# Kernel optimization log

Measured on AMD Instinct MI355X. Metric: run time of the kernel, lower is better.

The kernel has to match this reference:

```python
import jax, jax.numpy as jnp
import numpy as np

GROUP_SIZE = 128

def dequantize(imatrix, scales, zeros, group_size, out_dtype):
    # repeat group-wise scales/zeros along axis 0 to full weight shape
    rs = jnp.repeat(scales, group_size, axis=0)
    rz = jnp.repeat(zeros, group_size, axis=0)
    return ((imatrix.astype(rs.dtype) - rz.astype(rs.dtype)) * rs).astype(out_dtype)

def setup_inputs() -> dict:
    key = jax.random.key(0)
    ks = jax.random.split(key, 10)
    H, I, G = 4096, 14336, GROUP_SIZE
    B, S = 4, 2048
    x = jax.random.normal(ks[0], (B, S, H), dtype=jnp.float32)
    gate_w = jax.random.randint(ks[1], (H, I), 0, 16, dtype=jnp.int32)
    gate_z = jax.random.randint(ks[2], (H // G, I), 0, 16, dtype=jnp.int32)
    gate_s = jax.random.uniform(ks[3], (H // G, I), dtype=jnp.float32) * 0.01
    up_w = jax.random.randint(ks[4], (H, I), 0, 16, dtype=jnp.int32)
    up_z = jax.random.randint(ks[5], (H // G, I), 0, 16, dtype=jnp.int32)
    up_s = jax.random.uniform(ks[6], (H // G, I), dtype=jnp.float32) * 0.01
    down_w = jax.random.randint(ks[7], (I, H), 0, 16, dtype=jnp.int32)
    down_z = jax.random.randint(ks[8], (I // G, H), 0, 16, dtype=jnp.int32)
    down_s = jax.random.uniform(ks[9], (I // G, H), dtype=jnp.float32) * 0.01
    return {"x": x, "gate_w": gate_w, "gate_z": gate_z, "gate_s": gate_s,
            "up_w": up_w, "up_z": up_z, "up_s": up_s,
            "down_w": down_w, "down_z": down_z, "down_s": down_s}

def reference(x, gate_w, gate_z, gate_s, up_w, up_z, up_s, down_w, down_z, down_s):
    dt = x.dtype
    gate_proj = dequantize(gate_w, gate_s, gate_z, GROUP_SIZE, dt)  # [H, I]
    up_proj = dequantize(up_w, up_s, up_z, GROUP_SIZE, dt)          # [H, I]
    down_proj = dequantize(down_w, down_s, down_z, GROUP_SIZE, dt)  # [I, H]
    gate = jax.nn.silu(jnp.dot(x, gate_proj))  # [B, S, I]
    up = jnp.dot(x, up_proj)                   # [B, S, I]
    return jnp.dot(gate * up, down_proj)       # [B, S, H]
```

## Files before the change

### kernel.cpp

```cpp
#include <hip/hip_runtime.h>
#include <cstdint>
#include <cstddef>

typedef unsigned short u16;
typedef unsigned int u32;
typedef float f32x4 __attribute__((ext_vector_type(4)));
typedef __bf16 bf16x8 __attribute__((ext_vector_type(8)));

__device__ inline u16 f32_to_bf16(float f) {
  u32 u = __float_as_uint(f);
  u = (u + 0x7FFFu + ((u >> 16) & 1u)) >> 16;
  return (u16)u;
}

#define GLD16(src, dst)                                                        \
  __builtin_amdgcn_global_load_lds(                                            \
      (const __attribute__((address_space(1))) u32*)(src),                     \
      (__attribute__((address_space(3))) u32*)(dst), 16, 0, 0)

#define SBAR() __builtin_amdgcn_s_barrier()
#define SETPRIO(x) __builtin_amdgcn_s_setprio(x)
#define WAIT_LGKM0()                                                           \
  do {                                                                         \
    asm volatile("s_waitcnt lgkmcnt(0)" ::: "memory");                         \
    __builtin_amdgcn_sched_barrier(0);                                         \
  } while (0)
#define WAITV(N) asm volatile("s_waitcnt vmcnt(" #N ")" ::: "memory")
#define MFMA16(a, b, c) __builtin_amdgcn_mfma_f32_16x16x32_bf16(a, b, c, 0, 0, 0)

__device__ inline void stage_op(const char* src, void* ldsBase, int rowBase,
                                int wave) {
  GLD16(src, (char*)ldsBase + rowBase * 128 + wave * 1024);
}

__device__ inline bf16x8 fragK(const u16* tile, int row, int ks, int p) {
  const int byte = row * 128 + (((ks << 6) + (p << 4)) ^ ((row & 7) << 4));
  return *(const bf16x8*)((const char*)tile + byte);
}

__global__ void k_convert_x(const float* __restrict__ x, u16* __restrict__ o) {
  const long i = (long)blockIdx.x * 256 + threadIdx.x;
  const float4 a = ((const float4*)x)[i * 2];
  const float4 b = ((const float4*)x)[i * 2 + 1];
  uint4 r;
  r.x = (u32)f32_to_bf16(a.x) | ((u32)f32_to_bf16(a.y) << 16);
  r.y = (u32)f32_to_bf16(a.z) | ((u32)f32_to_bf16(a.w) << 16);
  r.z = (u32)f32_to_bf16(b.x) | ((u32)f32_to_bf16(b.y) << 16);
  r.w = (u32)f32_to_bf16(b.z) | ((u32)f32_to_bf16(b.w) << 16);
  ((uint4*)o)[i] = r;
}

__global__ __launch_bounds__(256) void k_dequant(const int* __restrict__ W,
                                                 const int* __restrict__ Z,
                                                 const float* __restrict__ S,
                                                 u16* __restrict__ out, int K,
                                                 int N) {
  __shared__ u16 ldsT[256 * 66];
  const int k0 = blockIdx.x * 64, n0 = blockIdx.y * 256;
  const int t = threadIdx.x;
  const int n4 = t & 63;
  const int kr = t >> 6;
  const int g = k0 >> 7;
  const int nb = n0 + n4 * 4;
  const int4 z4 = *(const int4*)(Z + (size_t)g * N + nb);
  const float4 s4 = *(const float4*)(S + (size_t)g * N + nb);
#pragma unroll
  for (int pass = 0; pass < 16; ++pass) {
    const int kl = kr + pass * 4;
    const int4 w4 = *(const int4*)(W + (size_t)(k0 + kl) * N + nb);
    ldsT[(n4 * 4 + 0) * 66 + kl] = f32_to_bf16((float)(w4.x - z4.x) * s4.x);
    ldsT[(n4 * 4 + 1) * 66 + kl] = f32_to_bf16((float)(w4.y - z4.y) * s4.y);
    ldsT[(n4 * 4 + 2) * 66 + kl] = f32_to_bf16((float)(w4.z - z4.z) * s4.z);
    ldsT[(n4 * 4 + 3) * 66 + kl] = f32_to_bf16((float)(w4.w - z4.w) * s4.w);
  }
  __syncthreads();
#pragma unroll
  for (int pass = 0; pass < 8; ++pass) {
    const int nl = pass * 32 + (t >> 3);
    const int kc = (t & 7) * 8;
    const u16* p = &ldsT[nl * 66 + kc];
    const u32 w0 = *(const u32*)(p + 0);
    const u32 w1 = *(const u32*)(p + 2);
    const u32 w2 = *(const u32*)(p + 4);
    const u32 w3 = *(const u32*)(p + 6);
    *(uint4*)(out + (size_t)(n0 + nl) * K + k0 + kc) =
        make_uint4(w0, w1, w2, w3);
  }
}

__global__ __launch_bounds__(512, 2) void k_gemm_gu(
    const u16* __restrict__ X, const u16* __restrict__ WG,
    const u16* __restrict__ WU, u16* __restrict__ Hout) {
  __shared__ __align__(16) u16 lA[2][16384];
  __shared__ __align__(16) u16 lG[2][8192];
  __shared__ __align__(16) u16 lU[2][8192];
  const int NT = 896;
  const int m0 = blockIdx.x * 256;
  const int ng = blockIdx.y;
  const int tid = threadIdx.x, lane = tid & 63, wave = tid >> 6;
  const int p = lane >> 4, r16 = lane & 15;
  const int wr = wave >> 2, wc = wave & 3;

  const int srow = tid >> 3;
  const int skb = (((tid ^ (tid >> 3)) & 7) << 4);
  const char* baA = (const char*)X + (long)(m0 + srow) * 8192 + skb;
  const char* baG = (const char*)WG + (long)srow * 8192 + skb;
  const char* baU = (const char*)WU + (long)srow * 8192 + skb;

#define NROW(t2) ((long)((ng + 8 * ((t2) >> 6)) << 7))
#define KBYTE(t2) (((t2) & 63) * 128)
#define ISS_A(t2, rb) \
  stage_op(baA + (long)(rb) * 8192 + KBYTE(t2), lA[(t2) & 1], rb, wave)
#define ISS_G(t2, rb) \
  stage_op(baG + (NROW(t2) + (rb)) * 8192 + KBYTE(t2), lG[(t2) & 1], rb, wave)
#define ISS_U(t2, rb) \
  stage_op(baU + (NROW(t2) + (rb)) * 8192 + KBYTE(t2), lU[(t2) & 1], rb, wave)

  f32x4 aG[8][2], aU[8][2];
  const f32x4 zero = {0.f, 0.f, 0.f, 0.f};
#pragma unroll
  for (int i = 0; i < 8; ++i)
#pragma unroll
    for (int j = 0; j < 2; ++j) {
      aG[i][j] = zero;
      aU[i][j] = zero;
    }

  ISS_A(0, 0); ISS_A(0, 128); ISS_G(0, 0); ISS_G(0, 64);
  ISS_U(0, 0); ISS_U(0, 64); ISS_A(0, 64); ISS_A(0, 192);
  ISS_A(1, 0); ISS_A(1, 128);
  WAITV(6);
  SBAR();

  for (int r = 0; r < 14; ++r) {
    for (int kt = 0; kt < 64; ++kt) {
      const int t = r * 64 + kt;
      const int b = kt & 1;
      const u16* hA = lA[b];
      const u16* hG = lG[b];
      const u16* hU = lU[b];
      bf16x8 af[2][4], gf[2][2], uf[2][2];
#pragma unroll
      for (int ks = 0; ks < 2; ++ks) {
#pragma unroll
        for (int ii = 0; ii < 4; ++ii)
          af[ks][ii] = fragK(hA, wr * 128 + ii * 16 + r16, ks, p);
#pragma unroll
        for (int j = 0; j < 2; ++j)
          gf[ks][j] = fragK(hG, wc * 32 + j * 16 + r16, ks, p);
      }
      if (t < NT - 1) { ISS_G(t + 1, 0); ISS_G(t + 1, 64); }
      SBAR();
      WAIT_LGKM0();
      SETPRIO(1);
#pragma unroll
      for (int ks = 0; ks < 2; ++ks)
#pragma unroll
        for (int ii = 0; ii < 4; ++ii)
#pragma unroll
          for (int j = 0; j < 2; ++j)
            aG[ii][j] = MFMA16(af[ks][ii], gf[ks][j], aG[ii][j]);
      SETPRIO(0);
      if (t < NT - 1) WAITV(6); else WAITV(2);
      SBAR();
#pragma unroll
      for (int ks = 0; ks < 2; ++ks)
#pragma unroll
        for (int j = 0; j < 2; ++j)
          uf[ks][j] = fragK(hU, wc * 32 + j * 16 + r16, ks, p);
      if (t < NT - 1) { ISS_U(t + 1, 0); ISS_U(t + 1, 64); }
      SBAR();
      WAIT_LGKM0();
      SETPRIO(1);
#pragma unroll
      for (int ks = 0; ks < 2; ++ks)
#pragma unroll
        for (int ii = 0; ii < 4; ++ii)
#pragma unroll
          for (int j = 0; j < 2; ++j)
            aU[ii][j] = MFMA16(af[ks][ii], uf[ks][j], aU[ii][j]);
      SETPRIO(0);
      if (t < NT - 1) WAITV(6); else WAITV(0);
      SBAR();
#pragma unroll
      for (int ks = 0; ks < 2; ++ks)
#pragma unroll
        for (int ii = 0; ii < 4; ++ii)
          af[ks][ii] = fragK(hA, wr * 128 + 64 + ii * 16 + r16, ks, p);
      if (t < NT - 1) { ISS_A(t + 1, 64); ISS_A(t + 1, 192); }
      SBAR();
      WAIT_LGKM0();
      SETPRIO(1);
#pragma unroll
      for (int ks = 0; ks < 2; ++ks)
#pragma unroll
        for (int ii = 0; ii < 4; ++ii)
#pragma unroll
          for (int j = 0; j < 2; ++j)
            aG[4 + ii][j] = MFMA16(af[ks][ii], gf[ks][j], aG[4 + ii][j]);
      SETPRIO(0);
      SBAR();
      if (t < NT - 2) { ISS_A(t + 2, 0); ISS_A(t + 2, 128); }
      SBAR();
      SETPRIO(1);
#pragma unroll
      for (int ks = 0; ks < 2; ++ks)
#pragma unroll
        for (int ii = 0; ii < 4; ++ii)
#pragma unroll
          for (int j = 0; j < 2; ++j)
            aU[4 + ii][j] = MFMA16(af[ks][ii], uf[ks][j], aU[4 + ii][j]);
      SETPRIO(0);
      if (t < NT - 2) WAITV(6);
      else if (t == NT - 2) WAITV(4);
      SBAR();
    }
    const int n0 = (ng + 8 * r) << 7;
#pragma unroll
    for (int i = 0; i < 8; ++i) {
      const int row = m0 + wr * 128 + i * 16 + p * 4;
#pragma unroll
      for (int j = 0; j < 2; ++j) {
        const int col = n0 + wc * 32 + j * 16 + r16;
        u16* dst = Hout + (size_t)row * 14336 + col;
#pragma unroll
        for (int rr = 0; rr < 4; ++rr) {
          const float gv = aG[i][j][rr], uv = aU[i][j][rr];
          const float sv = gv / (1.f + __expf(-gv)) * uv;
          dst[(size_t)rr * 14336] = f32_to_bf16(sv);
        }
      }
    }
#pragma unroll
    for (int i = 0; i < 8; ++i)
#pragma unroll
      for (int j = 0; j < 2; ++j) {
        aG[i][j] = zero;
        aU[i][j] = zero;
      }
  }
#undef ISS_A
#undef ISS_G
#undef ISS_U
#undef NROW
#undef KBYTE
}

__global__ __launch_bounds__(512, 2) void k_gemm_down(
    const u16* __restrict__ Hin, const u16* __restrict__ WD,
    float* __restrict__ Out) {
  __shared__ __align__(16) u16 lA[2][16384];
  __shared__ __align__(16) u16 lB[2][16384];
  const int NKT = 224;
  const int m0 = blockIdx.x * 256, n0 = blockIdx.y * 256;
  const int tid = threadIdx.x, lane = tid & 63, wave = tid >> 6;
  const int p = lane >> 4, r16 = lane & 15;
  const int wr = wave >> 2, wc = wave & 3;

  const int srow = tid >> 3;
  const int skb = (((tid ^ (tid >> 3)) & 7) << 4);
  const char* baA = (const char*)Hin + (long)(m0 + srow) * 28672 + skb;
  const char* baB = (const char*)WD + (long)(n0 + srow) * 28672 + skb;

#define ISS_A(kt2, rb) \
  stage_op(baA + (long)(rb) * 28672 + (long)(kt2) * 128, lA[(kt2) & 1], rb, wave)
#define ISS_B(kt2, rb) \
  stage_op(baB + (long)(rb) * 28672 + (long)(kt2) * 128, lB[(kt2) & 1], rb, wave)

  f32x4 acc[8][4];
  const f32x4 zero = {0.f, 0.f, 0.f, 0.f};
#pragma unroll
  for (int i = 0; i < 8; ++i)
#pragma unroll
    for (int j = 0; j < 4; ++j) acc[i][j] = zero;

  ISS_A(0, 0); ISS_A(0, 128); ISS_B(0, 0); ISS_B(0, 64);
  ISS_B(0, 128); ISS_B(0, 192); ISS_A(0, 64); ISS_A(0, 192);
  ISS_A(1, 0); ISS_A(1, 128);
  WAITV(4);
  SBAR();

  for (int kt = 0; kt < NKT; ++kt) {
    const int b = kt & 1;
    const u16* hA = lA[b];
    const u16* hB = lB[b];
    bf16x8 af[2][4], bfr[2][4];
#pragma unroll
    for (int ks = 0; ks < 2; ++ks) {
#pragma unroll
      for (int ii = 0; ii < 4; ++ii)
        af[ks][ii] = fragK(hA, wr * 128 + ii * 16 + r16, ks, p);
#pragma unroll
      for (int j = 0; j < 2; ++j)
        bfr[ks][j] = fragK(hB, wc * 64 + j * 16 + r16, ks, p);
    }
    if (kt < NKT - 1) { ISS_B(kt + 1, 0); ISS_B(kt + 1, 64); }
    SBAR();
    WAIT_LGKM0();
    SETPRIO(1);
#pragma unroll
    for (int ks = 0; ks < 2; ++ks)
#pragma unroll
      for (int ii = 0; ii < 4; ++ii)
#pragma unroll
        for (int j = 0; j < 2; ++j)
          acc[ii][j] = MFMA16(af[ks][ii], bfr[ks][j], acc[ii][j]);
    SETPRIO(0);
    SBAR();
#pragma unroll
    for (int ks = 0; ks < 2; ++ks)
#pragma unroll
      for (int j = 2; j < 4; ++j)
        bfr[ks][j] = fragK(hB, wc * 64 + j * 16 + r16, ks, p);
    if (kt < NKT - 1) { ISS_B(kt + 1, 128); ISS_B(kt + 1, 192); }
    SBAR();
    WAIT_LGKM0();
    SETPRIO(1);
#pragma unroll
    for (int ks = 0; ks < 2; ++ks)
#pragma unroll
      for (int ii = 0; ii < 4; ++ii)
#pragma unroll
        for (int j = 2; j < 4; ++j)
          acc[ii][j] = MFMA16(af[ks][ii], bfr[ks][j], acc[ii][j]);
    SETPRIO(0);
    if (kt < NKT - 1) WAITV(6); else WAITV(0);
    SBAR();
#pragma unroll
    for (int ks = 0; ks < 2; ++ks)
#pragma unroll
      for (int ii = 0; ii < 4; ++ii)
        af[ks][ii] = fragK(hA, wr * 128 + 64 + ii * 16 + r16, ks, p);
    if (kt < NKT - 1) { ISS_A(kt + 1, 64); ISS_A(kt + 1, 192); }
    SBAR();
    WAIT_LGKM0();
    SETPRIO(1);
#pragma unroll
    for (int ks = 0; ks < 2; ++ks)
#pragma unroll
      for (int ii = 0; ii < 4; ++ii)
#pragma unroll
        for (int j = 0; j < 2; ++j)
          acc[4 + ii][j] = MFMA16(af[ks][ii], bfr[ks][j], acc[4 + ii][j]);
    SETPRIO(0);
    SBAR();
    if (kt < NKT - 2) { ISS_A(kt + 2, 0); ISS_A(kt + 2, 128); }
    SBAR();
    SETPRIO(1);
#pragma unroll
    for (int ks = 0; ks < 2; ++ks)
#pragma unroll
      for (int ii = 0; ii < 4; ++ii)
#pragma unroll
        for (int j = 2; j < 4; ++j)
          acc[4 + ii][j] = MFMA16(af[ks][ii], bfr[ks][j], acc[4 + ii][j]);
    SETPRIO(0);
    if (kt < NKT - 2) WAITV(4);
    else if (kt == NKT - 2) WAITV(2);
    SBAR();
  }
#undef ISS_A
#undef ISS_B

#pragma unroll
  for (int i = 0; i < 8; ++i) {
    const int row = m0 + wr * 128 + i * 16 + p * 4;
#pragma unroll
    for (int j = 0; j < 4; ++j) {
      const int col = n0 + wc * 64 + j * 16 + r16;
      float* dst = Out + (size_t)row * 4096 + col;
#pragma unroll
      for (int r = 0; r < 4; ++r) dst[(size_t)r * 4096] = acc[i][j][r];
    }
  }
}

__global__ void k_fill(float* o, long n, float v) {
  const long i = (long)blockIdx.x * 256 + threadIdx.x;
  if (i < n) o[i] = v;
}

extern "C" void kernel_launch(void* const* d_in, const int* in_sizes, int n_in,
                              void* d_out, int out_size, void* d_ws,
                              size_t ws_size, hipStream_t stream) {
  const float* x = (const float*)d_in[0];
  const int* gw = (const int*)d_in[1];
  const int* gz = (const int*)d_in[2];
  const float* gs = (const float*)d_in[3];
  const int* uw = (const int*)d_in[4];
  const int* uz = (const int*)d_in[5];
  const float* us = (const float*)d_in[6];
  const int* dw = (const int*)d_in[7];
  const int* dz = (const int*)d_in[8];
  const float* dsc = (const float*)d_in[9];
  float* out = (float*)d_out;

  const size_t NX = 33554432UL, NW = 58720256UL;
  const size_t need = 2UL * (NX + 3UL * NW + 117440512UL);
  if (ws_size < need) {
    k_fill<<<(out_size + 255) / 256, 256, 0, stream>>>(out, out_size, 1.0e6f);
    return;
  }
  u16* wsx = (u16*)d_ws;
  u16* wgq = wsx + NX;
  u16* wuq = wgq + NW;
  u16* wdq = wuq + NW;
  u16* wh = wdq + NW;

  k_convert_x<<<16384, 256, 0, stream>>>(x, wsx);
  dim3 dq1(64, 56);
  k_dequant<<<dq1, 256, 0, stream>>>(gw, gz, gs, wgq, 4096, 14336);
  k_dequant<<<dq1, 256, 0, stream>>>(uw, uz, us, wuq, 4096, 14336);
  dim3 dq2(224, 16);
  k_dequant<<<dq2, 256, 0, stream>>>(dw, dz, dsc, wdq, 14336, 4096);
  dim3 g1(32, 8);
  k_gemm_gu<<<g1, 512, 0, stream>>>(wsx, wgq, wuq, wh);
  dim3 g2(32, 16);
  k_gemm_down<<<g2, 512, 0, stream>>>(wh, wdq, out);
}
```

Baseline: 2.688 ms.

## Restructure gate/up GEMM per-N-tile loop and prefetch next tile during epilogue

The gate/up GEMM's flattened 896-step pipeline becomes a per-N-tile 64-step loop with explicit base pointers. The prologue loads for the next N tile are issued before the SiLU*up epilogue stores, so global loads overlap the epilogue. A scheduling barrier pins this order. The vmcnt wait counts change (one mid-iteration wait is removed, others shift), which risks a race on the LDS buffers if the counts are wrong.

```diff
diff --git a/kernel.cpp b/kernel.cpp
--- a/kernel.cpp
+++ b/kernel.cpp
@@ -26,6 +26,7 @@
     __builtin_amdgcn_sched_barrier(0);                                         \
   } while (0)
 #define WAITV(N) asm volatile("s_waitcnt vmcnt(" #N ")" ::: "memory")
+#define SCHED_PIN() __builtin_amdgcn_sched_barrier(0)
 #define MFMA16(a, b, c) __builtin_amdgcn_mfma_f32_16x16x32_bf16(a, b, c, 0, 0, 0)
 
 __device__ inline void stage_op(const char* src, void* ldsBase, int rowBase,
@@ -94,7 +95,7 @@
   __shared__ __align__(16) u16 lA[2][16384];
   __shared__ __align__(16) u16 lG[2][8192];
   __shared__ __align__(16) u16 lU[2][8192];
-  const int NT = 896;
+  const int NKT = 64;
   const int m0 = blockIdx.x * 256;
   const int ng = blockIdx.y;
   const int tid = threadIdx.x, lane = tid & 63, wave = tid >> 6;
@@ -107,14 +108,20 @@
   const char* baG = (const char*)WG + (long)srow * 8192 + skb;
   const char* baU = (const char*)WU + (long)srow * 8192 + skb;
 
-#define NROW(t2) ((long)((ng + 8 * ((t2) >> 6)) << 7))
-#define KBYTE(t2) (((t2) & 63) * 128)
-#define ISS_A(t2, rb) \
-  stage_op(baA + (long)(rb) * 8192 + KBYTE(t2), lA[(t2) & 1], rb, wave)
-#define ISS_G(t2, rb) \
-  stage_op(baG + (NROW(t2) + (rb)) * 8192 + KBYTE(t2), lG[(t2) & 1], rb, wave)
-#define ISS_U(t2, rb) \
-  stage_op(baU + (NROW(t2) + (rb)) * 8192 + KBYTE(t2), lU[(t2) & 1], rb, wave)
+#define ISS_A(kt2, rb) \
+  stage_op(baA + (long)(rb) * 8192 + (long)(kt2) * 128, lA[(kt2) & 1], rb, wave)
+#define ISS_G(base, kt2, rb) \
+  stage_op((base) + (long)(rb) * 8192 + (long)(kt2) * 128, lG[(kt2) & 1], rb, wave)
+#define ISS_U(base, kt2, rb) \
+  stage_op((base) + (long)(rb) * 8192 + (long)(kt2) * 128, lU[(kt2) & 1], rb, wave)
+#define PROLOGUE(gG, gU)                                                       \
+  do {                                                                         \
+    ISS_A(0, 0); ISS_A(0, 128);                                                \
+    ISS_G(gG, 0, 0); ISS_G(gG, 0, 64);                                         \
+    ISS_U(gU, 0, 0); ISS_U(gU, 0, 64);                                         \
+    ISS_A(0, 64); ISS_A(0, 192);                                               \
+    ISS_A(1, 0); ISS_A(1, 128);                                                \
+  } while (0)
 
   f32x4 aG[8][2], aU[8][2];
   const f32x4 zero = {0.f, 0.f, 0.f, 0.f};
@@ -126,15 +133,15 @@
       aU[i][j] = zero;
     }
 
-  ISS_A(0, 0); ISS_A(0, 128); ISS_G(0, 0); ISS_G(0, 64);
-  ISS_U(0, 0); ISS_U(0, 64); ISS_A(0, 64); ISS_A(0, 192);
-  ISS_A(1, 0); ISS_A(1, 128);
-  WAITV(6);
-  SBAR();
+  const char* jbG = baG + (long)ng * 128 * 8192;
+  const char* jbU = baU + (long)ng * 128 * 8192;
+  PROLOGUE(jbG, jbU);
 
   for (int r = 0; r < 14; ++r) {
-    for (int kt = 0; kt < 64; ++kt) {
-      const int t = r * 64 + kt;
+    WAITV(4);
+    SBAR();
+
+    for (int kt = 0; kt < NKT; ++kt) {
       const int b = kt & 1;
       const u16* hA = lA[b];
       const u16* hG = lG[b];
@@ -149,7 +156,7 @@
         for (int j = 0; j < 2; ++j)
           gf[ks][j] = fragK(hG, wc * 32 + j * 16 + r16, ks, p);
       }
-      if (t < NT - 1) { ISS_G(t + 1, 0); ISS_G(t + 1, 64); }
+      if (kt < NKT - 1) { ISS_G(jbG, kt + 1, 0); ISS_G(jbG, kt + 1, 64); }
       SBAR();
       WAIT_LGKM0();
       SETPRIO(1);
@@ -161,14 +168,13 @@
           for (int j = 0; j < 2; ++j)
             aG[ii][j] = MFMA16(af[ks][ii], gf[ks][j], aG[ii][j]);
       SETPRIO(0);
-      if (t < NT - 1) WAITV(6); else WAITV(2);
       SBAR();
 #pragma unroll
       for (int ks = 0; ks < 2; ++ks)
 #pragma unroll
         for (int j = 0; j < 2; ++j)
           uf[ks][j] = fragK(hU, wc * 32 + j * 16 + r16, ks, p);
-      if (t < NT - 1) { ISS_U(t + 1, 0); ISS_U(t + 1, 64); }
+      if (kt < NKT - 1) { ISS_U(jbU, kt + 1, 0); ISS_U(jbU, kt + 1, 64); }
       SBAR();
       WAIT_LGKM0();
       SETPRIO(1);
@@ -180,14 +186,14 @@
           for (int j = 0; j < 2; ++j)
             aU[ii][j] = MFMA16(af[ks][ii], uf[ks][j], aU[ii][j]);
       SETPRIO(0);
-      if (t < NT - 1) WAITV(6); else WAITV(0);
+      if (kt < NKT - 1) WAITV(6); else WAITV(0);
       SBAR();
 #pragma unroll
       for (int ks = 0; ks < 2; ++ks)
 #pragma unroll
         for (int ii = 0; ii < 4; ++ii)
           af[ks][ii] = fragK(hA, wr * 128 + 64 + ii * 16 + r16, ks, p);
-      if (t < NT - 1) { ISS_A(t + 1, 64); ISS_A(t + 1, 192); }
+      if (kt < NKT - 1) { ISS_A(kt + 1, 64); ISS_A(kt + 1, 192); }
       SBAR();
       WAIT_LGKM0();
       SETPRIO(1);
@@ -200,7 +206,7 @@
             aG[4 + ii][j] = MFMA16(af[ks][ii], gf[ks][j], aG[4 + ii][j]);
       SETPRIO(0);
       SBAR();
-      if (t < NT - 2) { ISS_A(t + 2, 0); ISS_A(t + 2, 128); }
+      if (kt < NKT - 2) { ISS_A(kt + 2, 0); ISS_A(kt + 2, 128); }
       SBAR();
       SETPRIO(1);
 #pragma unroll
@@ -211,10 +217,16 @@
           for (int j = 0; j < 2; ++j)
             aU[4 + ii][j] = MFMA16(af[ks][ii], uf[ks][j], aU[4 + ii][j]);
       SETPRIO(0);
-      if (t < NT - 2) WAITV(6);
-      else if (t == NT - 2) WAITV(4);
+      if (kt < NKT - 2) WAITV(4);
+      else if (kt == NKT - 2) WAITV(2);
       SBAR();
     }
+
+    const char* nbG = baG + (long)(ng + 8 * (r + 1)) * 128 * 8192;
+    const char* nbU = baU + (long)(ng + 8 * (r + 1)) * 128 * 8192;
+    if (r < 13) PROLOGUE(nbG, nbU);
+    SCHED_PIN();
+
     const int n0 = (ng + 8 * r) << 7;
 #pragma unroll
     for (int i = 0; i < 8; ++i) {
@@ -231,6 +243,8 @@
         }
       }
     }
+    jbG = nbG;
+    jbU = nbU;
 #pragma unroll
     for (int i = 0; i < 8; ++i)
 #pragma unroll
@@ -242,8 +256,7 @@
 #undef ISS_A
 #undef ISS_G
 #undef ISS_U
-#undef NROW
-#undef KBYTE
+#undef PROLOGUE
 }
 
 __global__ __launch_bounds__(512, 2) void k_gemm_down(
```

After: 2.593 ms. 3.5% less time.
